# Performance work log

Measured on AMD Instinct MI355X. Metric: run time of the kernel, lower is better.

Reference implementation:

```python
import jax, jax.numpy as jnp
import numpy as np

B, S, D = 2, 2048, 1024
H = 16
HD = D // H
SCALE = float(np.sqrt(HD))


def setup_inputs() -> dict:
    key = jax.random.key(0)
    ks = jax.random.split(key, 10)
    def lin(k):
        # xavier_uniform for [out, in] = [D, D]
        bound = float(np.sqrt(6.0 / (D + D)))
        return jax.random.uniform(k, (D, D), jnp.float32, -bound, bound)
    return {
        "hidden_states": jax.random.normal(ks[0], (B, S, D), jnp.float32),
        "attention_mask": jnp.ones((B, S), jnp.float32),
        "Wq": lin(ks[1]), "bq": jnp.zeros((D,), jnp.float32),
        "Wk": lin(ks[2]), "bk": jnp.zeros((D,), jnp.float32),
        "Wv": lin(ks[3]), "bv": jnp.zeros((D,), jnp.float32),
        "Wo": lin(ks[4]), "bo": jnp.zeros((D,), jnp.float32),
    }


def _heads(x):
    # [B,S,D] -> [B,H,S,HD]
    return x.reshape(B, S, H, HD).transpose(0, 2, 1, 3)


def secure_softmax(scores):
    c = jnp.clip(scores, -3.0, 3.0)
    sig = 0.5 + 0.25 * c - 0.01 * c ** 3
    sig = jnp.clip(sig, 0.01, 0.99)
    return sig / (jnp.sum(sig, axis=-1, keepdims=True) + 1e-8)


def reference(hidden_states, attention_mask, Wq, bq, Wk, bk, Wv, bv, Wo, bo):
    q = _heads(hidden_states @ Wq.T + bq)
    k = _heads(hidden_states @ Wk.T + bk)
    v = _heads(hidden_states @ Wv.T + bv)
    # [B,H,S,S]
    scores = jnp.einsum("bhqd,bhkd->bhqk", q, k) / SCALE
    scores = scores + (1.0 - attention_mask[:, None, None, :]) * -10000.0
    probs = secure_softmax(scores)
    ctx = jnp.einsum("bhqk,bhkd->bhqd", probs, v)
    ctx = ctx.transpose(0, 2, 1, 3).reshape(B, S, D)
    return ctx @ Wo.T + bo
```

## Files before the change

kernel.cpp:

```cpp
#include <hip/hip_runtime.h>
#include <stdint.h>

#define B_ 2
#define S_ 2048
#define D_ 1024
#define H_ 16
#define HD_ 64
#define M_ (B_*S_)

typedef __bf16 bf16;
typedef __attribute__((ext_vector_type(8))) __bf16 bf16x8;
typedef __attribute__((ext_vector_type(4))) float f32x4;
typedef __attribute__((ext_vector_type(2))) float f32x2;

__device__ __forceinline__ void gload16(const bf16* g, bf16* l) {
    __builtin_amdgcn_global_load_lds(
        (const __attribute__((address_space(1))) void*)g,
        (__attribute__((address_space(3))) void*)l, 16, 0, 0);
}

__global__ void k_cvt_all(const float* __restrict__ hs,
                          const float* __restrict__ Wq, const float* __restrict__ Wk,
                          const float* __restrict__ Wv, const float* __restrict__ Wo,
                          bf16* __restrict__ hb,
                          bf16* __restrict__ wqb, bf16* __restrict__ wkb,
                          bf16* __restrict__ wvb, bf16* __restrict__ wob) {
    int blk = blockIdx.x;
    const float* s; bf16* d; int base;
    if (blk < 2048) { s = hs; d = hb; base = blk; }
    else {
        int r = blk - 2048; int which = r >> 9; base = r & 511;
        s = (which==0)?Wq:(which==1)?Wk:(which==2)?Wv:Wo;
        d = (which==0)?wqb:(which==1)?wkb:(which==2)?wvb:wob;
    }
    int idx = base*2048 + threadIdx.x*8;
    float4 a = *(const float4*)(s + idx);
    float4 b = *(const float4*)(s + idx + 4);
    bf16 o[8] = {(bf16)a.x,(bf16)a.y,(bf16)a.z,(bf16)a.w,
                 (bf16)b.x,(bf16)b.y,(bf16)b.z,(bf16)b.w};
    *(int4*)(d + idx) = *(const int4*)o;
}

__global__ __launch_bounds__(256) void k_gemm_qkv(
    const bf16* __restrict__ X,
    const bf16* __restrict__ Wq, const bf16* __restrict__ Wk, const bf16* __restrict__ Wv,
    const float* __restrict__ bq, const float* __restrict__ bk, const float* __restrict__ bv,
    bf16* __restrict__ Qo, bf16* __restrict__ Ko, bf16* __restrict__ Vo)
{
    const int hh = blockIdx.x;
    const int n0 = hh * 64;
    const int m0 = blockIdx.y * 128;
    const int t = threadIdx.x;
    const int w = t >> 6, lane = t & 63, quad = lane >> 4, l15 = lane & 15;
    const int lr = lane >> 3;
    const int lc = (lane & 7) ^ lr;
    const int sx = l15 & 7;
    const int mw = (w >> 1) * 64, nw = (w & 1) * 32;

    __shared__ __align__(16) char smraw[40960];
    bf16* As  = (bf16*)smraw;
    bf16* Bsf = (bf16*)(smraw + 16384);
    bf16* epi = (bf16*)smraw;

    f32x4 acc[3][4][2];
    #pragma unroll
    for (int z = 0; z < 3; z++)
        #pragma unroll
        for (int i = 0; i < 4; i++)
            #pragma unroll
            for (int j = 0; j < 2; j++)
                acc[z][i][j] = (f32x4){0.f,0.f,0.f,0.f};

    const bf16* gA = X + (size_t)(m0 + w*8 + lr)*D_ + lc*8;
    const bf16* Wz[3] = {Wq, Wk, Wv};
    const bf16* gB[6];
    #pragma unroll
    for (int cc = 0; cc < 6; cc++) {
        const int z = cc >> 1;
        const int rowz = (cc & 1)*32 + w*8 + lr;
        gB[cc] = Wz[z] + (size_t)(n0 + rowz)*D_ + lc*8;
    }

    for (int k0 = 0; k0 < D_; k0 += 64) {
        #pragma unroll
        for (int c = 0; c < 4; c++)
            gload16(gA + (size_t)c*32*D_ + k0, &As[c*2048 + w*512]);
        #pragma unroll
        for (int cc = 0; cc < 6; cc++)
            gload16(gB[cc] + k0, &Bsf[cc*2048 + w*512]);
        __syncthreads();
        #pragma unroll
        for (int ks = 0; ks < 2; ks++) {
            bf16x8 af[4], bfr[3][2];
            #pragma unroll
            for (int i = 0; i < 4; i++)
                af[i] = *(const bf16x8*)&As[(mw + i*16 + l15)*64 + (((ks*4+quad)^sx)*8)];
            #pragma unroll
            for (int z = 0; z < 3; z++)
                #pragma unroll
                for (int j = 0; j < 2; j++)
                    bfr[z][j] = *(const bf16x8*)&Bsf[z*4096 + (nw + j*16 + l15)*64 + (((ks*4+quad)^sx)*8)];
            #pragma unroll
            for (int z = 0; z < 3; z++)
                #pragma unroll
                for (int i = 0; i < 4; i++)
                    #pragma unroll
                    for (int j = 0; j < 2; j++)
                        acc[z][i][j] = __builtin_amdgcn_mfma_f32_16x16x32_bf16(af[i], bfr[z][j], acc[z][i][j], 0, 0, 0);
        }
        __syncthreads();
    }

    #pragma unroll
    for (int z = 0; z < 2; z++) {
        const float scale = z ? 1.0f : 0.125f;
        const float* bias = z ? bk : bq;
        bf16* Out = z ? Ko : Qo;
        #pragma unroll
        for (int j = 0; j < 2; j++) {
            int n = nw + j*16 + l15;
            float bn = bias[n0 + n];
            #pragma unroll
            for (int i = 0; i < 4; i++) {
                int mloc = mw + i*16 + quad*4;
                #pragma unroll
                for (int r = 0; r < 4; r++)
                    epi[(mloc + r)*72 + n] = (bf16)((acc[z][i][j][r] + bn) * scale);
            }
        }
        __syncthreads();
        #pragma unroll
        for (int p = 0; p < 4; p++) {
            int c = t + 256*p;
            int row = c >> 3;
            int ncol = (c & 7) * 8;
            int4 val = *(const int4*)&epi[row*72 + ncol];
            int m = m0 + row; int bb = m >> 11, s = m & 2047;
            *(int4*)&Out[((size_t)((bb*H_ + hh)*S_ + s))*HD_ + ncol] = val;
        }
        __syncthreads();
    }
    {
        #pragma unroll
        for (int j = 0; j < 2; j++) {
            int n = nw + j*16 + l15;
            float bn = bv[n0 + n];
            #pragma unroll
            for (int i = 0; i < 4; i++) {
                int mloc = mw + i*16 + quad*4;
                union { bf16 h4[4]; uint2 u; } pk;
                #pragma unroll
                for (int r = 0; r < 4; r++) pk.h4[r] = (bf16)(acc[2][i][j][r] + bn);
                *(uint2*)&epi[n*136 + mloc] = pk.u;
            }
        }
        __syncthreads();
        #pragma unroll
        for (int p = 0; p < 4; p++) {
            int c = t + 256*p;
            int row = c >> 4;
            int mcol = (c & 15) * 8;
            int4 val = *(const int4*)&epi[row*136 + mcol];
            int m = m0 + mcol; int bb = m >> 11, s = m & 2047;
            *(int4*)&Vo[((size_t)((bb*H_ + hh)*HD_ + row))*S_ + s] = val;
        }
    }
}

__global__ __launch_bounds__(256) void k_gemm_out(
    const bf16* __restrict__ X, const bf16* __restrict__ W,
    const float* __restrict__ bias, float* __restrict__ Out)
{
    const int n0 = blockIdx.x * 128;
    const int m0 = blockIdx.y * 64;
    const int t = threadIdx.x;
    const int w = t >> 6, lane = t & 63, quad = lane >> 4, l15 = lane & 15;
    const int lr = lane >> 3;
    const int lc = (lane & 7) ^ lr;
    const int sx = l15 & 7;
    const int nw = w * 32;

    __shared__ __align__(16) bf16 As[64*64];
    __shared__ __align__(16) bf16 Bs[128*64];

    f32x4 acc[4][2];
    #pragma unroll
    for (int i = 0; i < 4; i++)
        #pragma unroll
        for (int j = 0; j < 2; j++)
            acc[i][j] = (f32x4){0.f,0.f,0.f,0.f};

    const bf16* gA = X + (size_t)(m0 + w*8 + lr)*D_ + lc*8;
    const bf16* gB = W + (size_t)(n0 + w*8 + lr)*D_ + lc*8;

    for (int k0 = 0; k0 < D_; k0 += 64) {
        #pragma unroll
        for (int c = 0; c < 2; c++)
            gload16(gA + (size_t)c*32*D_ + k0, &As[c*2048 + w*512]);
        #pragma unroll
        for (int c = 0; c < 4; c++)
            gload16(gB + (size_t)c*32*D_ + k0, &Bs[c*2048 + w*512]);
        __syncthreads();
        #pragma unroll
        for (int ks = 0; ks < 2; ks++) {
            bf16x8 af[4], bfr[2];
            #pragma unroll
            for (int i = 0; i < 4; i++)
                af[i] = *(const bf16x8*)&As[(i*16 + l15)*64 + (((ks*4+quad)^sx)*8)];
            #pragma unroll
            for (int j = 0; j < 2; j++)
                bfr[j] = *(const bf16x8*)&Bs[(nw + j*16 + l15)*64 + (((ks*4+quad)^sx)*8)];
            #pragma unroll
            for (int i = 0; i < 4; i++)
                #pragma unroll
                for (int j = 0; j < 2; j++)
                    acc[i][j] = __builtin_amdgcn_mfma_f32_16x16x32_bf16(af[i], bfr[j], acc[i][j], 0, 0, 0);
        }
        __syncthreads();
    }

    #pragma unroll
    for (int j = 0; j < 2; j++) {
        int n = n0 + nw + j*16 + l15;
        float bn = bias[n];
        #pragma unroll
        for (int i = 0; i < 4; i++) {
            int mbase = m0 + i*16 + quad*4;
            #pragma unroll
            for (int r = 0; r < 4; r++)
                Out[(size_t)(mbase + r)*D_ + n] = acc[i][j][r] + bn;
        }
    }
}

#define ATT_PAIR(BUFA, K0, PF)                                                  \
  {                                                                             \
    if (PF) {                                                                   \
      const int kp = (K0) + 128;                                                \
      _Pragma("unroll")                                                         \
      for (int c = 0; c < 2; c++) {                                             \
        gload16(KstK + (size_t)(kp + c*32)*HD_,      &Ks[(BUFA)^2][c*2048 + w*512]);     \
        gload16(VstV + (size_t)c*32*S_ + kp,         &Vs[(BUFA)^2][c*2048 + w*512]);     \
        gload16(KstK + (size_t)(kp + 64 + c*32)*HD_, &Ks[((BUFA)^2)+1][c*2048 + w*512]); \
        gload16(VstV + (size_t)c*32*S_ + kp + 64,    &Vs[((BUFA)^2)+1][c*2048 + w*512]); \
      }                                                                         \
    }                                                                           \
    f32x4 st[2][4][2];                                                          \
    _Pragma("unroll")                                                           \
    for (int sub = 0; sub < 2; sub++) {                                         \
      const int kb = (K0) + sub*64;                                             \
      _Pragma("unroll")                                                         \
      for (int g = 0; g < 4; g++) {                                             \
        float4 m4 = *(const float4*)&Ms[kb + quad*8 + (g>>1)*32 + (g&1)*4];     \
        f32x4 sti = (f32x4){m4.x, m4.y, m4.z, m4.w} * 10000.f - 10000.f;        \
        st[sub][g][0] = sti;                                                    \
        st[sub][g][1] = sti;                                                    \
      }                                                                         \
    }                                                                           \
    __builtin_amdgcn_s_setprio(1);                                              \
    _Pragma("unroll")                                                           \
    for (int sub = 0; sub < 2; sub++) {                                         \
      _Pragma("unroll")                                                         \
      for (int ks = 0; ks < 2; ks++) {                                          \
        _Pragma("unroll")                                                       \
        for (int g = 0; g < 4; g++) {                                           \
          const int kk = g >> 1, hf = g & 1;                                    \
          bf16x8 af = *(const bf16x8*)&Ks[(BUFA)+sub][(arow + hf*4 + kk*32)*64 + (((ks*4+quad)^sx)*8)]; \
          _Pragma("unroll")                                                     \
          for (int m2 = 0; m2 < 2; m2++)                                        \
            st[sub][g][m2] = __builtin_amdgcn_mfma_f32_16x16x32_bf16(af, qf[m2][ks], st[sub][g][m2], 0, 0, 0); \
        }                                                                       \
      }                                                                         \
    }                                                                           \
    __builtin_amdgcn_s_setprio(0);                                              \
    _Pragma("unroll")                                                           \
    for (int sub = 0; sub < 2; sub++) {                                         \
      bf16x8 pa[2][2];                                                          \
      _Pragma("unroll")                                                         \
      for (int m2 = 0; m2 < 2; m2++) {                                          \
        _Pragma("unroll")                                                       \
        for (int kk = 0; kk < 2; kk++) {                                        \
          union { bf16 h8[8]; bf16x8 v; } pk;                                   \
          _Pragma("unroll")                                                     \
          for (int hf = 0; hf < 2; hf++) {                                      \
            f32x4 sv = st[sub][kk*2 + hf][m2];                                  \
            f32x2 lo, hi;                                                       \
            lo.x = __builtin_amdgcn_fmed3f(sv[0], -3.f, 3.f);                   \
            lo.y = __builtin_amdgcn_fmed3f(sv[1], -3.f, 3.f);                   \
            hi.x = __builtin_amdgcn_fmed3f(sv[2], -3.f, 3.f);                   \
            hi.y = __builtin_amdgcn_fmed3f(sv[3], -3.f, 3.f);                   \
            f32x2 tlo = lo * lo * (-0.01f) + 0.25f;                             \
            f32x2 thi = hi * hi * (-0.01f) + 0.25f;                             \
            f32x2 slo = lo * tlo + 0.5f;                                        \
            f32x2 shi = hi * thi + 0.5f;                                        \
            lacv[m2] += slo;                                                    \
            lacv[m2] += shi;                                                    \
            pk.h8[hf*4+0] = (bf16)slo.x; pk.h8[hf*4+1] = (bf16)slo.y;           \
            pk.h8[hf*4+2] = (bf16)shi.x; pk.h8[hf*4+3] = (bf16)shi.y;           \
          }                                                                     \
          pa[m2][kk] = pk.v;                                                    \
        }                                                                       \
      }                                                                         \
      _Pragma("unroll")                                                         \
      for (int kk = 0; kk < 2; kk++) {                                          \
        bf16x8 vf[4];                                                           \
        _Pragma("unroll")                                                       \
        for (int nt = 0; nt < 4; nt++)                                          \
          vf[nt] = *(const bf16x8*)&Vs[(BUFA)+sub][(nt*16 + l15)*64 + (((kk*4+quad)^sx)*8)]; \
        __builtin_amdgcn_s_setprio(1);                                          \
        _Pragma("unroll")                                                       \
        for (int m2 = 0; m2 < 2; m2++)                                          \
          _Pragma("unroll")                                                     \
          for (int nt = 0; nt < 4; nt++)                                        \
            cacc[m2][nt] = __builtin_amdgcn_mfma_f32_16x16x32_bf16(pa[m2][kk], vf[nt], cacc[m2][nt], 0, 0, 0); \
        __builtin_amdgcn_s_setprio(0);                                          \
      }                                                                         \
    }                                                                           \
    asm volatile("s_waitcnt vmcnt(0)\n\ts_barrier" ::: "memory");               \
  }

__global__ __launch_bounds__(256, 2) void k_attn(
    const bf16* __restrict__ Q, const bf16* __restrict__ K, const bf16* __restrict__ Vt,
    const float* __restrict__ mask, bf16* __restrict__ Ctx)
{
    const int bh = blockIdx.y;
    const int b = bh >> 4, h = bh & 15;
    const int q0 = blockIdx.x * 128;
    const int t = threadIdx.x;
    const int w = t >> 6, lane = t & 63, quad = lane >> 4, l15 = lane & 15;
    const int lr = lane >> 3;
    const int lcV = (lane & 7) ^ lr;
    const int lcK = (lane & 7) ^ ((lr & 3) | ((w & 1) << 2));
    const int sx = l15 & 7;
    const int arow = ((l15 & 12) << 1) | (l15 & 3);

    __shared__ __align__(16) bf16 Ks[4][64*64];
    __shared__ __align__(16) bf16 Vs[4][64*64];
    __shared__ __align__(16) float Ms[S_];

    bf16x8 qf[2][2];
    const bf16* Qbase = Q + ((size_t)bh*S_ + q0 + w*32)*HD_;
    #pragma unroll
    for (int m2 = 0; m2 < 2; m2++)
        #pragma unroll
        for (int ks = 0; ks < 2; ks++)
            qf[m2][ks] = *(const bf16x8*)&Qbase[(size_t)(m2*16 + l15)*HD_ + ks*32 + quad*8];

    f32x4 cacc[2][4];
    #pragma unroll
    for (int i = 0; i < 2; i++)
        #pragma unroll
        for (int j = 0; j < 4; j++)
            cacc[i][j] = (f32x4){0.f,0.f,0.f,0.f};
    f32x2 lacv[2];
    #pragma unroll
    for (int m2 = 0; m2 < 2; m2++) lacv[m2] = (f32x2){0.f,0.f};

    const bf16* KstK = K  + ((size_t)bh*S_  + w*8 + lr)*HD_ + lcK*8;
    const bf16* VstV = Vt + ((size_t)bh*HD_ + w*8 + lr)*S_  + lcV*8;

    {
        const float* mg = mask + (size_t)b*S_ + t*8;
        float4 a0 = *(const float4*)mg;
        float4 a1 = *(const float4*)(mg + 4);
        *(float4*)&Ms[t*8]     = a0;
        *(float4*)&Ms[t*8 + 4] = a1;
    }
    #pragma unroll
    for (int c = 0; c < 2; c++) {
        gload16(KstK + (size_t)(c*32)*HD_,      &Ks[0][c*2048 + w*512]);
        gload16(VstV + (size_t)c*32*S_,         &Vs[0][c*2048 + w*512]);
        gload16(KstK + (size_t)(64 + c*32)*HD_, &Ks[1][c*2048 + w*512]);
        gload16(VstV + (size_t)c*32*S_ + 64,    &Vs[1][c*2048 + w*512]);
    }
    asm volatile("s_waitcnt vmcnt(0) lgkmcnt(0)\n\ts_barrier" ::: "memory");

    for (int q2 = 0; q2 < S_/256; q2++) {
        const int k0 = q2 * 256;
        ATT_PAIR(0, k0,        true);
        ATT_PAIR(2, k0 + 128,  (q2 < S_/256 - 1));
    }

    float s[2];
    #pragma unroll
    for (int m2 = 0; m2 < 2; m2++) {
        float v = lacv[m2].x + lacv[m2].y;
        v += __shfl_xor(v, 16);
        v += __shfl_xor(v, 32);
        s[m2] = v;
    }

    #pragma unroll
    for (int m2 = 0; m2 < 2; m2++) {
        #pragma unroll
        for (int r = 0; r < 4; r++) {
            float rs = __shfl(s[m2], quad*4 + r);
            float rinv = 1.0f / (rs + 1e-8f);
            size_t row = (size_t)(b*S_ + q0 + w*32 + m2*16 + quad*4 + r);
            #pragma unroll
            for (int nt = 0; nt < 4; nt++)
                Ctx[row*D_ + h*HD_ + nt*16 + l15] = (bf16)(cacc[m2][nt][r] * rinv);
        }
    }
}

extern "C" void kernel_launch(void* const* d_in, const int* in_sizes, int n_in,
                              void* d_out, int out_size, void* d_ws, size_t ws_size,
                              hipStream_t stream) {
    const float* hs   = (const float*)d_in[0];
    const float* mask = (const float*)d_in[1];
    const float* Wq   = (const float*)d_in[2];
    const float* bq   = (const float*)d_in[3];
    const float* Wk   = (const float*)d_in[4];
    const float* bk   = (const float*)d_in[5];
    const float* Wv   = (const float*)d_in[6];
    const float* bv   = (const float*)d_in[7];
    const float* Wo   = (const float*)d_in[8];
    const float* bo   = (const float*)d_in[9];
    float* out = (float*)d_out;

    char* ws = (char*)d_ws;
    const size_t MB = 1024*1024;
    bf16* hb   = (bf16*)(ws);
    bf16* wqb  = (bf16*)(ws + 8*MB);
    bf16* wkb  = (bf16*)(ws + 10*MB);
    bf16* wvb  = (bf16*)(ws + 12*MB);
    bf16* wob  = (bf16*)(ws + 14*MB);
    bf16* qb   = (bf16*)(ws + 16*MB);
    bf16* kb   = (bf16*)(ws + 24*MB);
    bf16* vtb  = (bf16*)(ws + 32*MB);
    bf16* ctxb = (bf16*)(ws + 40*MB);

    k_cvt_all<<<2048 + 4*512, 256, 0, stream>>>(hs, Wq, Wk, Wv, Wo, hb, wqb, wkb, wvb, wob);

    k_gemm_qkv<<<dim3(H_, M_/128), 256, 0, stream>>>(
        hb, wqb, wkb, wvb, bq, bk, bv, qb, kb, vtb);

    k_attn<<<dim3(S_/128, B_*H_), 256, 0, stream>>>(qb, kb, vtb, mask, ctxb);

    k_gemm_out<<<dim3(D_/128, M_/64), 256, 0, stream>>>(ctxb, wob, bo, out);
}
```

Baseline: 183.7 us.

## Double-buffer LDS tiles in QKV and output projection GEMMs

Both projection GEMMs now keep two LDS buffers and prefetch the next K-tile with global_load_lds while MFMAs run on the current tile, using one waitcnt+barrier per iteration instead of two syncthreads. MFMA blocks are also wrapped in s_setprio to favour compute waves. The goal is to hide global-to-LDS load latency behind compute. The cost is doubled LDS use (80KB for QKV, 48KB for out), which may lower occupancy.

```diff
diff --git a/kernel.cpp b/kernel.cpp
--- a/kernel.cpp
+++ b/kernel.cpp
@@ -57,9 +57,7 @@
     const int sx = l15 & 7;
     const int mw = (w >> 1) * 64, nw = (w & 1) * 32;
 
-    __shared__ __align__(16) char smraw[40960];
-    bf16* As  = (bf16*)smraw;
-    bf16* Bsf = (bf16*)(smraw + 16384);
+    __shared__ __align__(16) char smraw[81920];
     bf16* epi = (bf16*)smraw;
 
     f32x4 acc[3][4][2];
@@ -81,14 +79,36 @@
         gB[cc] = Wz[z] + (size_t)(n0 + rowz)*D_ + lc*8;
     }
 
-    for (int k0 = 0; k0 < D_; k0 += 64) {
+    {
+        bf16* As  = (bf16*)smraw;
+        bf16* Bsf = (bf16*)(smraw + 16384);
         #pragma unroll
         for (int c = 0; c < 4; c++)
-            gload16(gA + (size_t)c*32*D_ + k0, &As[c*2048 + w*512]);
+            gload16(gA + (size_t)c*32*D_, &As[c*2048 + w*512]);
         #pragma unroll
         for (int cc = 0; cc < 6; cc++)
-            gload16(gB[cc] + k0, &Bsf[cc*2048 + w*512]);
-        __syncthreads();
+            gload16(gB[cc], &Bsf[cc*2048 + w*512]);
+    }
+    asm volatile("s_waitcnt vmcnt(0)\n\ts_barrier" ::: "memory");
+
+    for (int it = 0; it < 16; it++) {
+        const int k0 = it * 64;
+        char* base = smraw + (size_t)(it & 1) * 40960;
+        bf16* As  = (bf16*)base;
+        bf16* Bsf = (bf16*)(base + 16384);
+
+        if (it < 15) {
+            char* nb = smraw + (size_t)((it + 1) & 1) * 40960;
+            bf16* Asn = (bf16*)nb;
+            bf16* Bsn = (bf16*)(nb + 16384);
+            #pragma unroll
+            for (int c = 0; c < 4; c++)
+                gload16(gA + (size_t)c*32*D_ + k0 + 64, &Asn[c*2048 + w*512]);
+            #pragma unroll
+            for (int cc = 0; cc < 6; cc++)
+                gload16(gB[cc] + k0 + 64, &Bsn[cc*2048 + w*512]);
+        }
+
         #pragma unroll
         for (int ks = 0; ks < 2; ks++) {
             bf16x8 af[4], bfr[3][2];
@@ -100,6 +120,7 @@
                 #pragma unroll
                 for (int j = 0; j < 2; j++)
                     bfr[z][j] = *(const bf16x8*)&Bsf[z*4096 + (nw + j*16 + l15)*64 + (((ks*4+quad)^sx)*8)];
+            __builtin_amdgcn_s_setprio(1);
             #pragma unroll
             for (int z = 0; z < 3; z++)
                 #pragma unroll
@@ -107,8 +128,10 @@
                     #pragma unroll
                     for (int j = 0; j < 2; j++)
                         acc[z][i][j] = __builtin_amdgcn_mfma_f32_16x16x32_bf16(af[i], bfr[z][j], acc[z][i][j], 0, 0, 0);
-        }
-        __syncthreads();
+            __builtin_amdgcn_s_setprio(0);
+        }
+
+        asm volatile("s_waitcnt vmcnt(0)\n\ts_barrier" ::: "memory");
     }
 
     #pragma unroll
@@ -180,8 +203,7 @@
     const int sx = l15 & 7;
     const int nw = w * 32;
 
-    __shared__ __align__(16) bf16 As[64*64];
-    __shared__ __align__(16) bf16 Bs[128*64];
+    __shared__ __align__(16) char smem[49152];
 
     f32x4 acc[4][2];
     #pragma unroll
@@ -193,14 +215,36 @@
     const bf16* gA = X + (size_t)(m0 + w*8 + lr)*D_ + lc*8;
     const bf16* gB = W + (size_t)(n0 + w*8 + lr)*D_ + lc*8;
 
-    for (int k0 = 0; k0 < D_; k0 += 64) {
+    {
+        bf16* As = (bf16*)smem;
+        bf16* Bs = (bf16*)(smem + 8192);
         #pragma unroll
         for (int c = 0; c < 2; c++)
-            gload16(gA + (size_t)c*32*D_ + k0, &As[c*2048 + w*512]);
+            gload16(gA + (size_t)c*32*D_, &As[c*2048 + w*512]);
         #pragma unroll
         for (int c = 0; c < 4; c++)
-            gload16(gB + (size_t)c*32*D_ + k0, &Bs[c*2048 + w*512]);
-        __syncthreads();
+            gload16(gB + (size_t)c*32*D_, &Bs[c*2048 + w*512]);
+    }
+    asm volatile("s_waitcnt vmcnt(0)\n\ts_barrier" ::: "memory");
+
+    for (int it = 0; it < 16; it++) {
+        const int k0 = it * 64;
+        char* base = smem + (size_t)(it & 1) * 24576;
+        bf16* As = (bf16*)base;
+        bf16* Bs = (bf16*)(base + 8192);
+
+        if (it < 15) {
+            char* nb = smem + (size_t)((it + 1) & 1) * 24576;
+            bf16* Asn = (bf16*)nb;
+            bf16* Bsn = (bf16*)(nb + 8192);
+            #pragma unroll
+            for (int c = 0; c < 2; c++)
+                gload16(gA + (size_t)c*32*D_ + k0 + 64, &Asn[c*2048 + w*512]);
+            #pragma unroll
+            for (int c = 0; c < 4; c++)
+                gload16(gB + (size_t)c*32*D_ + k0 + 64, &Bsn[c*2048 + w*512]);
+        }
+
         #pragma unroll
         for (int ks = 0; ks < 2; ks++) {
             bf16x8 af[4], bfr[2];
@@ -210,13 +254,16 @@
             #pragma unroll
             for (int j = 0; j < 2; j++)
                 bfr[j] = *(const bf16x8*)&Bs[(nw + j*16 + l15)*64 + (((ks*4+quad)^sx)*8)];
+            __builtin_amdgcn_s_setprio(1);
             #pragma unroll
             for (int i = 0; i < 4; i++)
                 #pragma unroll
                 for (int j = 0; j < 2; j++)
                     acc[i][j] = __builtin_amdgcn_mfma_f32_16x16x32_bf16(af[i], bfr[j], acc[i][j], 0, 0, 0);
-        }
-        __syncthreads();
+            __builtin_amdgcn_s_setprio(0);
+        }
+
+        asm volatile("s_waitcnt vmcnt(0)\n\ts_barrier" ::: "memory");
     }
 
     #pragma unroll
```

After: 192.1 us. +4.6%, slower.
